# Performance work log

Hardware: AMD Instinct MI355X
Metric: run time of the kernel (lower is better)

The kernel has to match this reference:

```python
import jax, jax.numpy as jnp
import numpy as np

B, O, K, GS = 4096, 11008, 4096, 128  # batch, out_features, in_features, group_size
G = K // GS  # num groups = 32


def _unpack_int4(packed):
    """packed: [N, K//2] int values in [0,256) holding two 4-bit nibbles (low first).
    Returns signed int4 values as float32 [N, K]."""
    low = packed & 15
    high = (packed >> 4) & 15
    q = jnp.stack([low, high], axis=-1).reshape(packed.shape[0], -1)  # interleave low,high
    return jnp.where(q >= 8, q - 16, q).astype(jnp.float32)


def setup_inputs() -> dict:
    key = jax.random.key(0)
    k1, k2, k3, k4, k5 = jax.random.split(key, 5)
    x = jax.random.randint(k1, (B, K // 2), 0, 256, dtype=jnp.int32)
    a_scale = jax.random.uniform(k2, (B, G), dtype=jnp.float32).astype(jnp.float16)
    w_packed = jax.random.randint(k3, (O, K // 2), 0, 256, dtype=jnp.int32)
    w_scale = jax.random.uniform(k4, (O, G), dtype=jnp.float32).astype(jnp.float16)
    bias = (jax.random.normal(k5, (O,), dtype=jnp.float32) * 0.02).astype(jnp.float16)
    return {"x": x, "a_scale": a_scale, "w_packed": w_packed, "w_scale": w_scale,
            "bias": bias, "group_size": GS}


def reference(x, a_scale, w_packed, w_scale, bias, group_size):
    # out[b,o] = sum_g a_scale[b,g] * w_scale[o,g] * sum_{k in g} x_int4[b,k] * w_int4[o,k] + bias[o]
    # Fold the per-group scales into the dequantized operands, then a single GEMM
    # (mathematically identical to group-wise int accumulate + dequant).
    b, o = x.shape[0], w_packed.shape[0]
    k = x.shape[1] * 2
    g = k // group_size
    xq = _unpack_int4(x).reshape(b, g, group_size) * a_scale.astype(jnp.float32)[:, :, None]
    wq = _unpack_int4(w_packed).reshape(o, g, group_size) * w_scale.astype(jnp.float32)[:, :, None]
    out = jnp.einsum('bgk,ogk->bo', xq, wq).astype(jnp.float16)  # [B, O] fp16
    return out + bias
```

## Files before the change

kernel.cpp:

```cpp
#include <hip/hip_runtime.h>
#include <hip/hip_bf16.h>


#define B_DIM 4096
#define O_DIM 11008
#define K_DIM 4096
#define G_NUM 32

#define NX4 2097152u
#define NW4 5636096u
#define X8_BYTES  16777216u
#define W8_BYTES  45088768u

typedef int   i32x4 __attribute__((ext_vector_type(4)));
typedef float f32x4 __attribute__((ext_vector_type(4)));

__device__ __forceinline__ unsigned pack2(int v) {
    int t = v ^ 0x88;
    unsigned lo = (unsigned)(((t & 15) - 8) & 0xFF);
    unsigned hi = (unsigned)((((t >> 4) & 15) - 8) & 0xFF);
    return lo | (hi << 8);
}

__global__ __launch_bounds__(256)
void unpack_kernel(const int* __restrict__ xq, const int* __restrict__ wq,
                   unsigned char* __restrict__ X8, unsigned char* __restrict__ W8) {
    unsigned idx = blockIdx.x * 256u + threadIdx.x;
    const int* src;
    unsigned char* dst;
    if (idx < NX4) {
        src = xq + (size_t)idx * 4;
        dst = X8 + (size_t)idx * 8;
    } else {
        unsigned j = idx - NX4;
        src = wq + (size_t)j * 4;
        dst = W8 + (size_t)j * 8;
    }
    int4 v = *(const int4*)src;
    unsigned r0 = pack2(v.x) | (pack2(v.y) << 16);
    unsigned r1 = pack2(v.z) | (pack2(v.w) << 16);
    uint2 o; o.x = r0; o.y = r1;
    *(uint2*)dst = o;
}

__global__ __launch_bounds__(256)
void tscale_kernel(const float* __restrict__ as_, const float* __restrict__ ws_,
                   float* __restrict__ asT, float* __restrict__ wsT) {
    int bx = blockIdx.x, g = blockIdx.y, t = threadIdx.x;
    if (bx < 16) {
        int b = bx * 256 + t;
        asT[g * B_DIM + b] = as_[(size_t)b * G_NUM + g];
    } else {
        int o = (bx - 16) * 256 + t;
        wsT[(size_t)g * O_DIM + o] = ws_[(size_t)o * G_NUM + g];
    }
}

__global__ __launch_bounds__(256, 2)
void gemm_i8(const unsigned char* __restrict__ X8, const unsigned char* __restrict__ W8,
             const float* __restrict__ asT, const float* __restrict__ wsT,
             const float* __restrict__ bias, float* __restrict__ out) {
    __shared__ __align__(16) unsigned char A8[128 * 128];
    __shared__ __align__(16) unsigned char B8[128 * 128];

    const int tid  = threadIdx.x;
    const int wv   = tid >> 6;
    const int lane = tid & 63;
    const int quad = lane >> 4;
    const int lq   = lane & 15;
    const int bm   = blockIdx.x;
    const int bn   = blockIdx.y;
    const int wm   = (wv & 1) << 6;
    const int wn   = (wv >> 1) << 6;

    f32x4 facc[4][4] = {};

    const int l8 = lane >> 3;
    const int c8 = lane & 7;
    const int sw_chunk = ((c8 ^ l8) << 4);
    const size_t xrow0 = (size_t)(bm * 128) * K_DIM;
    const size_t wrow0 = (size_t)(bn * 128) * K_DIM;

    for (int g = 0; g < G_NUM; ++g) {
        const int gb = g << 7;

#pragma unroll
        for (int s = 0; s < 4; ++s) {
            const int slab = (wv << 2) + s;
            const int row  = (slab << 3) + l8;
            const unsigned char* gpA = X8 + xrow0 + (size_t)row * K_DIM + gb + sw_chunk;
            const unsigned char* gpB = W8 + wrow0 + (size_t)row * K_DIM + gb + sw_chunk;
            __builtin_amdgcn_global_load_lds(
                (const __attribute__((address_space(1))) void*)gpA,
                (__attribute__((address_space(3))) void*)(A8 + (slab << 10)), 16, 0, 0);
            __builtin_amdgcn_global_load_lds(
                (const __attribute__((address_space(1))) void*)gpB,
                (__attribute__((address_space(3))) void*)(B8 + (slab << 10)), 16, 0, 0);
        }
        __syncthreads();

        i32x4 gacc[4][4] = {};
#pragma unroll
        for (int ks = 0; ks < 2; ++ks) {
            i32x4 av[4], bv[4];
            const int pa = ((((ks << 2) + quad) ^ (lq & 7)) << 4);
#pragma unroll
            for (int i = 0; i < 4; ++i) {
                av[i] = *(const i32x4*)&A8[((wm + (i << 4) + lq) << 7) + pa];
                bv[i] = *(const i32x4*)&B8[((wn + (i << 4) + lq) << 7) + pa];
            }
#pragma unroll
            for (int i = 0; i < 4; ++i)
#pragma unroll
                for (int j = 0; j < 4; ++j)
                    gacc[i][j] = __builtin_amdgcn_mfma_i32_16x16x64_i8(av[i], bv[j], gacc[i][j], 0, 0, 0);
        }

        f32x4 asr[4];
        float wsn[4];
#pragma unroll
        for (int i = 0; i < 4; ++i)
            asr[i] = *(const f32x4*)&asT[(g << 12) + bm * 128 + wm + (i << 4) + (quad << 2)];
#pragma unroll
        for (int j = 0; j < 4; ++j)
            wsn[j] = wsT[(size_t)g * O_DIM + bn * 128 + wn + (j << 4) + lq];
#pragma unroll
        for (int i = 0; i < 4; ++i)
#pragma unroll
            for (int j = 0; j < 4; ++j)
#pragma unroll
                for (int r = 0; r < 4; ++r)
                    facc[i][j][r] += (asr[i][r] * wsn[j]) * (float)gacc[i][j][r];

        __syncthreads();
    }

    const int n0 = bn * 128 + wn + lq;
    const int m0 = bm * 128 + wm + (quad << 2);
    float bvs[4];
#pragma unroll
    for (int j = 0; j < 4; ++j) bvs[j] = bias[n0 + (j << 4)];
#pragma unroll
    for (int i = 0; i < 4; ++i) {
#pragma unroll
        for (int r = 0; r < 4; ++r) {
            float* orow = out + (size_t)(m0 + (i << 4) + r) * O_DIM;
#pragma unroll
            for (int j = 0; j < 4; ++j)
                orow[n0 + (j << 4)] = facc[i][j][r] + bvs[j];
        }
    }
}

extern "C" void kernel_launch(void* const* d_in, const int* in_sizes, int n_in,
                              void* d_out, int out_size, void* d_ws, size_t ws_size,
                              hipStream_t stream) {
    const int*   xq   = (const int*)d_in[0];
    const float* as_  = (const float*)d_in[1];
    const int*   wq   = (const int*)d_in[2];
    const float* ws_  = (const float*)d_in[3];
    const float* bias = (const float*)d_in[4];
    float* out        = (float*)d_out;

    unsigned char* X8 = (unsigned char*)d_ws;
    unsigned char* W8 = X8 + X8_BYTES;
    float* asT = (float*)((unsigned char*)d_ws + X8_BYTES + W8_BYTES);
    float* wsT = asT + (size_t)G_NUM * B_DIM;

    unpack_kernel<<<(NX4 + NW4) / 256, 256, 0, stream>>>(xq, wq, X8, W8);
    tscale_kernel<<<dim3(59, 32), 256, 0, stream>>>(as_, ws_, asT, wsT);
    gemm_i8<<<dim3(B_DIM / 128, O_DIM / 128), 256, 0, stream>>>(X8, W8, asT, wsT, bias, out);
}
```

Before: 533.7 us.

## Double-buffer LDS tiles in int8 GEMM and widen unpack per thread

The GEMM now keeps two LDS buffers for the A and B tiles. It issues the asynchronous global-to-LDS loads for group g+1 before the MFMA work on group g, which also drops one barrier per iteration. The aim is to hide global-load latency behind the matrix math, at the cost of twice the LDS per block, which could limit occupancy. The unpack kernel now converts 8 packed ints per thread with 16-byte stores instead of 4 ints with 8-byte stores, cutting thread count and widening memory transactions. The scale accumulation uses an explicit fma.

Result: slower. 613.4 us (+14.9%).

```diff
diff --git a/kernel.cpp b/kernel.cpp
--- a/kernel.cpp
+++ b/kernel.cpp
@@ -7,8 +7,8 @@
 #define K_DIM 4096
 #define G_NUM 32
 
-#define NX4 2097152u
-#define NW4 5636096u
+#define NX32 8388608u
+#define NW32 22544384u
 #define X8_BYTES  16777216u
 #define W8_BYTES  45088768u
 
@@ -25,22 +25,25 @@
 __global__ __launch_bounds__(256)
 void unpack_kernel(const int* __restrict__ xq, const int* __restrict__ wq,
                    unsigned char* __restrict__ X8, unsigned char* __restrict__ W8) {
-    unsigned idx = blockIdx.x * 256u + threadIdx.x;
+    unsigned t = blockIdx.x * 256u + threadIdx.x;
     const int* src;
     unsigned char* dst;
-    if (idx < NX4) {
-        src = xq + (size_t)idx * 4;
-        dst = X8 + (size_t)idx * 8;
+    if (t < NX32 / 8) {
+        src = xq + (size_t)t * 8;
+        dst = X8 + (size_t)t * 16;
     } else {
-        unsigned j = idx - NX4;
-        src = wq + (size_t)j * 4;
-        dst = W8 + (size_t)j * 8;
+        unsigned j = t - NX32 / 8;
+        src = wq + (size_t)j * 8;
+        dst = W8 + (size_t)j * 16;
     }
-    int4 v = *(const int4*)src;
-    unsigned r0 = pack2(v.x) | (pack2(v.y) << 16);
-    unsigned r1 = pack2(v.z) | (pack2(v.w) << 16);
-    uint2 o; o.x = r0; o.y = r1;
-    *(uint2*)dst = o;
+    int4 v0 = ((const int4*)src)[0];
+    int4 v1 = ((const int4*)src)[1];
+    uint4 o;
+    o.x = pack2(v0.x) | (pack2(v0.y) << 16);
+    o.y = pack2(v0.z) | (pack2(v0.w) << 16);
+    o.z = pack2(v1.x) | (pack2(v1.y) << 16);
+    o.w = pack2(v1.z) | (pack2(v1.w) << 16);
+    *(uint4*)dst = o;
 }
 
 __global__ __launch_bounds__(256)
@@ -60,8 +63,8 @@
 void gemm_i8(const unsigned char* __restrict__ X8, const unsigned char* __restrict__ W8,
              const float* __restrict__ asT, const float* __restrict__ wsT,
              const float* __restrict__ bias, float* __restrict__ out) {
-    __shared__ __align__(16) unsigned char A8[128 * 128];
-    __shared__ __align__(16) unsigned char B8[128 * 128];
+    __shared__ __align__(16) unsigned char A8[2][16384];
+    __shared__ __align__(16) unsigned char B8[2][16384];
 
     const int tid  = threadIdx.x;
     const int wv   = tid >> 6;
@@ -81,9 +84,8 @@
     const size_t xrow0 = (size_t)(bm * 128) * K_DIM;
     const size_t wrow0 = (size_t)(bn * 128) * K_DIM;
 
-    for (int g = 0; g < G_NUM; ++g) {
+    auto stage = [&](int g, int buf) {
         const int gb = g << 7;
-
 #pragma unroll
         for (int s = 0; s < 4; ++s) {
             const int slab = (wv << 2) + s;
@@ -92,29 +94,17 @@
             const unsigned char* gpB = W8 + wrow0 + (size_t)row * K_DIM + gb + sw_chunk;
             __builtin_amdgcn_global_load_lds(
                 (const __attribute__((address_space(1))) void*)gpA,
-                (__attribute__((address_space(3))) void*)(A8 + (slab << 10)), 16, 0, 0);
+                (__attribute__((address_space(3))) void*)(&A8[buf][0] + (slab << 10)), 16, 0, 0);
             __builtin_amdgcn_global_load_lds(
                 (const __attribute__((address_space(1))) void*)gpB,
-                (__attribute__((address_space(3))) void*)(B8 + (slab << 10)), 16, 0, 0);
+                (__attribute__((address_space(3))) void*)(&B8[buf][0] + (slab << 10)), 16, 0, 0);
         }
-        __syncthreads();
+    };
 
-        i32x4 gacc[4][4] = {};
-#pragma unroll
-        for (int ks = 0; ks < 2; ++ks) {
-            i32x4 av[4], bv[4];
-            const int pa = ((((ks << 2) + quad) ^ (lq & 7)) << 4);
-#pragma unroll
-            for (int i = 0; i < 4; ++i) {
-                av[i] = *(const i32x4*)&A8[((wm + (i << 4) + lq) << 7) + pa];
-                bv[i] = *(const i32x4*)&B8[((wn + (i << 4) + lq) << 7) + pa];
-            }
-#pragma unroll
-            for (int i = 0; i < 4; ++i)
-#pragma unroll
-                for (int j = 0; j < 4; ++j)
-                    gacc[i][j] = __builtin_amdgcn_mfma_i32_16x16x64_i8(av[i], bv[j], gacc[i][j], 0, 0, 0);
-        }
+    stage(0, 0);
+
+    for (int g = 0; g < G_NUM; ++g) {
+        const int buf = g & 1;
 
         f32x4 asr[4];
         float wsn[4];
@@ -124,15 +114,35 @@
 #pragma unroll
         for (int j = 0; j < 4; ++j)
             wsn[j] = wsT[(size_t)g * O_DIM + bn * 128 + wn + (j << 4) + lq];
+
+        __syncthreads();
+
+        if (g + 1 < G_NUM) stage(g + 1, buf ^ 1);
+
+        i32x4 gacc[4][4] = {};
+#pragma unroll
+        for (int ks = 0; ks < 2; ++ks) {
+            i32x4 av[4], bv[4];
+            const int pa = ((((ks << 2) + quad) ^ (lq & 7)) << 4);
+#pragma unroll
+            for (int i = 0; i < 4; ++i) {
+                av[i] = *(const i32x4*)&A8[buf][((wm + (i << 4) + lq) << 7) + pa];
+                bv[i] = *(const i32x4*)&B8[buf][((wn + (i << 4) + lq) << 7) + pa];
+            }
+#pragma unroll
+            for (int i = 0; i < 4; ++i)
+#pragma unroll
+                for (int j = 0; j < 4; ++j)
+                    gacc[i][j] = __builtin_amdgcn_mfma_i32_16x16x64_i8(av[i], bv[j], gacc[i][j], 0, 0, 0);
+        }
+
 #pragma unroll
         for (int i = 0; i < 4; ++i)
 #pragma unroll
             for (int j = 0; j < 4; ++j)
 #pragma unroll
                 for (int r = 0; r < 4; ++r)
-                    facc[i][j][r] += (asr[i][r] * wsn[j]) * (float)gacc[i][j][r];
-
-        __syncthreads();
+                    facc[i][j][r] = __builtin_fmaf(asr[i][r] * wsn[j], (float)gacc[i][j][r], facc[i][j][r]);
     }
 
     const int n0 = bn * 128 + wn + lq;
@@ -167,7 +177,7 @@
     float* asT = (float*)((unsigned char*)d_ws + X8_BYTES + W8_BYTES);
     float* wsT = asT + (size_t)G_NUM * B_DIM;
 
-    unpack_kernel<<<(NX4 + NW4) / 256, 256, 0, stream>>>(xq, wq, X8, W8);
+    unpack_kernel<<<(NX32 + NW32) / 8 / 256, 256, 0, stream>>>(xq, wq, X8, W8);
     tscale_kernel<<<dim3(59, 32), 256, 0, stream>>>(as_, ws_, asT, wsT);
     gemm_i8<<<dim3(B_DIM / 128, O_DIM / 128), 256, 0, stream>>>(X8, W8, asT, wsT, bias, out);
 }
```
